# Kernel tuning notes

Hardware: AMD Instinct MI355X
Metric: run time of the kernel (lower is better)

Reference implementation:

```python
import jax, jax.numpy as jnp
import numpy as np

B = 131072  # batch of states
D = 32      # input/hidden width (hardcoded in Policy)
L = 40      # number of hidden layers

def setup_inputs() -> dict:
    key = jax.random.key(0)
    k1, k2, k3, k4, k5 = jax.random.split(key, 5)
    scale = 1.0 / np.sqrt(D)  # ~ torch Linear init scale
    return {
        "state": jax.random.normal(k1, (B, D), dtype=jnp.float32),
        "W_hidden": jax.random.normal(k2, (L, D, D), dtype=jnp.float32) * scale,
        "b_hidden": jax.random.normal(k3, (L, D), dtype=jnp.float32) * scale,
        "W_out": jax.random.normal(k4, (1, D), dtype=jnp.float32) * scale,
        "b_out": jax.random.normal(k5, (1,), dtype=jnp.float32) * scale,
    }

def reference(state, W_hidden, b_hidden, W_out, b_out):
    # torch Linear: y = x @ W.T + b, with W of shape [out, in].
    def layer(x, wb):
        w, b = wb
        return jax.nn.relu(jnp.einsum('bi,oi->bo', x, w) + b), None
    x, _ = jax.lax.scan(layer, state, (W_hidden, b_hidden))
    # final Linear(32, 1), no activation
    return jnp.einsum('bi,oi->bo', x, W_out) + b_out  # [B, 1]
```

## Files before the change

### kernel.cpp

```cpp
#include <hip/hip_runtime.h>


#define NB 131072
#define DD 32
#define NL 40
#define BIAS_BYTES ((NL + 1) * 32 * 4)
#define WTAB_OFF   BIAS_BYTES
#define WTAB_BYTES ((NL + 1) * 4 * 64 * 16)
#define LDS_LAYERS 18
#define LDS_BYTES  (BIAS_BYTES + LDS_LAYERS * 4096)

typedef short bf16x8 __attribute__((ext_vector_type(8)));
typedef float f32x4 __attribute__((ext_vector_type(4)));

union Frag { int4 q; int i[4]; bf16x8 v; };
union BFrag { float4 q; f32x4 v; };

__device__ inline unsigned f2bf(float f) {
  unsigned u = __float_as_uint(f);
  return (u + 0x7fffu + ((u >> 16) & 1u)) >> 16;
}
__device__ inline float bf2f(unsigned s) { return __int_as_float((int)(s << 16)); }

__global__ __launch_bounds__(64) void build_tables(
    const float* __restrict__ Wh, const float* __restrict__ bh,
    const float* __restrict__ Wout, const float* __restrict__ bout,
    char* __restrict__ ws) {
  const int l = blockIdx.x;
  const int lane = threadIdx.x;
  const int m = lane & 15, g = lane >> 4;
  int4* wtab = (int4*)(ws + WTAB_OFF);
  float* bc = (float*)ws;
  for (int p = 0; p < 4; ++p) {
    const int row = (p & 1) ? (16 + m) : m;
    const bool lopart = (p >= 2);
    int wds[4];
    for (int w = 0; w < 4; ++w) {
      unsigned wd = 0;
      for (int e = 0; e < 2; ++e) {
        const int j = 2 * w + e;
        const int k = (j < 4) ? (4 * g + j) : (16 + 4 * g + (j - 4));
        float v;
        if (l < NL) v = Wh[(l * 32 + row) * 32 + k];
        else        v = (row == 0) ? Wout[k] : 0.f;
        unsigned hi = f2bf(v);
        unsigned val = lopart ? f2bf(v - bf2f(hi)) : hi;
        wd |= val << (16 * e);
      }
      wds[w] = (int)wd;
    }
    wtab[(l * 4 + p) * 64 + lane] = make_int4(wds[0], wds[1], wds[2], wds[3]);
  }
  if (lane < 32) {
    float bv = (l < NL) ? bh[l * 32 + lane] : ((lane == 0) ? bout[0] : 0.f);
    bc[l * 32 + lane] = bv;
  }
}

__device__ inline void split2(float a, float b, int& hi, int& lo) {
  const unsigned ia = __float_as_uint(a), ib = __float_as_uint(b);
  hi = (int)__builtin_amdgcn_perm(ia, ib, 0x03020706u);
  const float ha = __int_as_float((int)(ia & 0xffff0000u));
  const float hb = __int_as_float((int)(ib & 0xffff0000u));
  const float la = a - ha, lb = b - hb;
  lo = (int)__builtin_amdgcn_perm(__float_as_uint(la), __float_as_uint(lb),
                                  0x03020706u);
}

#define MFMA16(A, B, C) __builtin_amdgcn_mfma_f32_16x16x32_bf16((A), (B), (C), 0, 0, 0)

__global__ __launch_bounds__(1024, 8) void policy_mfma(
    const float* __restrict__ state, const char* __restrict__ tab,
    float* __restrict__ out) {
  extern __shared__ char smem[];
  const int tid = threadIdx.x;
  const int lane = tid & 63;
  const int n = lane & 15, g = lane >> 4;
  const int wid = blockIdx.x * 16 + (tid >> 6);
  const int bbase = wid * 16;

  {
    const int4* src = (const int4*)tab;
    int4* dst = (int4*)smem;
    for (int i = tid; i < LDS_BYTES / 16; i += 1024) dst[i] = src[i];
  }

  Frag bhi, blo;
  {
    const float* xr = state + (size_t)(bbase + n) * DD;
    float4 xa = *(const float4*)(xr + 4 * g);
    float4 xc = *(const float4*)(xr + 16 + 4 * g);
    split2(xa.x, xa.y, bhi.i[0], blo.i[0]);
    split2(xa.z, xa.w, bhi.i[1], blo.i[1]);
    split2(xc.x, xc.y, bhi.i[2], blo.i[2]);
    split2(xc.z, xc.w, bhi.i[3], blo.i[3]);
  }

  __syncthreads();

  const int4* lw = (const int4*)(smem + WTAB_OFF) + lane;
  const float* bc = (const float*)smem;
  const int4* gw = (const int4*)(tab + WTAB_OFF) + lane;

  auto layer = [&](int l, const int4* __restrict__ WP, int lofs) {
    Frag w0h, w1h, w0l, w1l;
    w0h.q = WP[lofs * 256 + 0];
    w1h.q = WP[lofs * 256 + 64];
    w0l.q = WP[lofs * 256 + 128];
    w1l.q = WP[lofs * 256 + 192];
    BFrag c0, c1;
    c0.q = *(const float4*)(bc + l * 32 + 4 * g);
    c1.q = *(const float4*)(bc + l * 32 + 16 + 4 * g);

    f32x4 a0 = MFMA16(w0h.v, bhi.v, c0.v);
    f32x4 a1 = MFMA16(w1h.v, bhi.v, c1.v);
    a0 = MFMA16(w0l.v, bhi.v, a0);
    a1 = MFMA16(w1l.v, bhi.v, a1);
    a0 = MFMA16(w0h.v, blo.v, a0);
    a1 = MFMA16(w1h.v, blo.v, a1);

    split2(fmaxf(a0[0], 0.f), fmaxf(a0[1], 0.f), bhi.i[0], blo.i[0]);
    split2(fmaxf(a0[2], 0.f), fmaxf(a0[3], 0.f), bhi.i[1], blo.i[1]);
    split2(fmaxf(a1[0], 0.f), fmaxf(a1[1], 0.f), bhi.i[2], blo.i[2]);
    split2(fmaxf(a1[2], 0.f), fmaxf(a1[3], 0.f), bhi.i[3], blo.i[3]);
  };

#pragma unroll
  for (int l = 0; l < LDS_LAYERS; ++l) layer(l, lw, l);
#pragma unroll
  for (int l = LDS_LAYERS; l < NL; ++l) layer(l, gw, l);

  float res;
  {
    Frag w0h, w0l;
    w0h.q = gw[NL * 256 + 0];
    w0l.q = gw[NL * 256 + 128];
    BFrag c0;
    c0.q = *(const float4*)(bc + NL * 32 + 4 * g);
    f32x4 a0 = MFMA16(w0h.v, bhi.v, c0.v);
    a0 = MFMA16(w0l.v, bhi.v, a0);
    a0 = MFMA16(w0h.v, blo.v, a0);
    res = a0[0];
  }

  if (lane < 16) out[bbase + n] = res;
}

extern "C" void kernel_launch(void* const* d_in, const int* in_sizes, int n_in,
                              void* d_out, int out_size, void* d_ws, size_t ws_size,
                              hipStream_t stream) {
  const float* state = (const float*)d_in[0];
  const float* Wh    = (const float*)d_in[1];
  const float* bh    = (const float*)d_in[2];
  const float* Wout  = (const float*)d_in[3];
  const float* bout  = (const float*)d_in[4];
  float* out = (float*)d_out;

  build_tables<<<NL + 1, 64, 0, stream>>>(Wh, bh, Wout, bout, (char*)d_ws);

  policy_mfma<<<512, 1024, LDS_BYTES, stream>>>(state, (const char*)d_ws, out);
}
```

Before: 46.59 us.

## Process four 16-row tiles per wave and stage more layers in LDS

```diff
diff --git a/kernel.cpp b/kernel.cpp
--- a/kernel.cpp
+++ b/kernel.cpp
@@ -7,7 +7,7 @@
 #define BIAS_BYTES ((NL + 1) * 32 * 4)
 #define WTAB_OFF   BIAS_BYTES
 #define WTAB_BYTES ((NL + 1) * 4 * 64 * 16)
-#define LDS_LAYERS 18
+#define LDS_LAYERS 38
 #define LDS_BYTES  (BIAS_BYTES + LDS_LAYERS * 4096)
 
 typedef short bf16x8 __attribute__((ext_vector_type(8)));
@@ -69,31 +69,32 @@
 
 #define MFMA16(A, B, C) __builtin_amdgcn_mfma_f32_16x16x32_bf16((A), (B), (C), 0, 0, 0)
 
-__global__ __launch_bounds__(1024, 8) void policy_mfma(
+__global__ __launch_bounds__(512, 2) void policy_mfma(
     const float* __restrict__ state, const char* __restrict__ tab,
     float* __restrict__ out) {
   extern __shared__ char smem[];
   const int tid = threadIdx.x;
   const int lane = tid & 63;
   const int n = lane & 15, g = lane >> 4;
-  const int wid = blockIdx.x * 16 + (tid >> 6);
-  const int bbase = wid * 16;
+  const int wid = blockIdx.x * 8 + (tid >> 6);
+  const int bbase = wid * 64;
 
   {
     const int4* src = (const int4*)tab;
     int4* dst = (int4*)smem;
-    for (int i = tid; i < LDS_BYTES / 16; i += 1024) dst[i] = src[i];
+    for (int i = tid; i < LDS_BYTES / 16; i += 512) dst[i] = src[i];
   }
 
-  Frag bhi, blo;
-  {
-    const float* xr = state + (size_t)(bbase + n) * DD;
+  Frag bhi[4], blo[4];
+#pragma unroll
+  for (int t = 0; t < 4; ++t) {
+    const float* xr = state + (size_t)(bbase + 16 * t + n) * DD;
     float4 xa = *(const float4*)(xr + 4 * g);
     float4 xc = *(const float4*)(xr + 16 + 4 * g);
-    split2(xa.x, xa.y, bhi.i[0], blo.i[0]);
-    split2(xa.z, xa.w, bhi.i[1], blo.i[1]);
-    split2(xc.x, xc.y, bhi.i[2], blo.i[2]);
-    split2(xc.z, xc.w, bhi.i[3], blo.i[3]);
+    split2(xa.x, xa.y, bhi[t].i[0], blo[t].i[0]);
+    split2(xa.z, xa.w, bhi[t].i[1], blo[t].i[1]);
+    split2(xc.x, xc.y, bhi[t].i[2], blo[t].i[2]);
+    split2(xc.z, xc.w, bhi[t].i[3], blo[t].i[3]);
   }
 
   __syncthreads();
@@ -102,48 +103,63 @@
   const float* bc = (const float*)smem;
   const int4* gw = (const int4*)(tab + WTAB_OFF) + lane;
 
-  auto layer = [&](int l, const int4* __restrict__ WP, int lofs) {
+#pragma unroll
+  for (int l = 0; l < NL; ++l) {
     Frag w0h, w1h, w0l, w1l;
-    w0h.q = WP[lofs * 256 + 0];
-    w1h.q = WP[lofs * 256 + 64];
-    w0l.q = WP[lofs * 256 + 128];
-    w1l.q = WP[lofs * 256 + 192];
+    const int4* WP = (l < LDS_LAYERS) ? lw : gw;
+    w0h.q = WP[l * 256 + 0];
+    w1h.q = WP[l * 256 + 64];
+    w0l.q = WP[l * 256 + 128];
+    w1l.q = WP[l * 256 + 192];
     BFrag c0, c1;
     c0.q = *(const float4*)(bc + l * 32 + 4 * g);
     c1.q = *(const float4*)(bc + l * 32 + 16 + 4 * g);
 
-    f32x4 a0 = MFMA16(w0h.v, bhi.v, c0.v);
-    f32x4 a1 = MFMA16(w1h.v, bhi.v, c1.v);
-    a0 = MFMA16(w0l.v, bhi.v, a0);
-    a1 = MFMA16(w1l.v, bhi.v, a1);
-    a0 = MFMA16(w0h.v, blo.v, a0);
-    a1 = MFMA16(w1h.v, blo.v, a1);
-
-    split2(fmaxf(a0[0], 0.f), fmaxf(a0[1], 0.f), bhi.i[0], blo.i[0]);
-    split2(fmaxf(a0[2], 0.f), fmaxf(a0[3], 0.f), bhi.i[1], blo.i[1]);
-    split2(fmaxf(a1[0], 0.f), fmaxf(a1[1], 0.f), bhi.i[2], blo.i[2]);
-    split2(fmaxf(a1[2], 0.f), fmaxf(a1[3], 0.f), bhi.i[3], blo.i[3]);
-  };
+    f32x4 a0[4], a1[4];
+#pragma unroll
+    for (int t = 0; t < 4; ++t) a0[t] = MFMA16(w0h.v, bhi[t].v, c0.v);
+#pragma unroll
+    for (int t = 0; t < 4; ++t) a1[t] = MFMA16(w1h.v, bhi[t].v, c1.v);
+#pragma unroll
+    for (int t = 0; t < 4; ++t) a0[t] = MFMA16(w0l.v, bhi[t].v, a0[t]);
+#pragma unroll
+    for (int t = 0; t < 4; ++t) a1[t] = MFMA16(w1l.v, bhi[t].v, a1[t]);
+#pragma unroll
+    for (int t = 0; t < 4; ++t) a0[t] = MFMA16(w0h.v, blo[t].v, a0[t]);
+#pragma unroll
+    for (int t = 0; t < 4; ++t) a1[t] = MFMA16(w1h.v, blo[t].v, a1[t]);
 
 #pragma unroll
-  for (int l = 0; l < LDS_LAYERS; ++l) layer(l, lw, l);
-#pragma unroll
-  for (int l = LDS_LAYERS; l < NL; ++l) layer(l, gw, l);
+    for (int t = 0; t < 4; ++t) {
+      split2(fmaxf(a0[t][0], 0.f), fmaxf(a0[t][1], 0.f), bhi[t].i[0], blo[t].i[0]);
+      split2(fmaxf(a0[t][2], 0.f), fmaxf(a0[t][3], 0.f), bhi[t].i[1], blo[t].i[1]);
+      split2(fmaxf(a1[t][0], 0.f), fmaxf(a1[t][1], 0.f), bhi[t].i[2], blo[t].i[2]);
+      split2(fmaxf(a1[t][2], 0.f), fmaxf(a1[t][3], 0.f), bhi[t].i[3], blo[t].i[3]);
+    }
+  }
 
-  float res;
+  float res[4];
   {
     Frag w0h, w0l;
     w0h.q = gw[NL * 256 + 0];
     w0l.q = gw[NL * 256 + 128];
     BFrag c0;
     c0.q = *(const float4*)(bc + NL * 32 + 4 * g);
-    f32x4 a0 = MFMA16(w0h.v, bhi.v, c0.v);
-    a0 = MFMA16(w0l.v, bhi.v, a0);
-    a0 = MFMA16(w0h.v, blo.v, a0);
-    res = a0[0];
+    f32x4 a0[4];
+#pragma unroll
+    for (int t = 0; t < 4; ++t) a0[t] = MFMA16(w0h.v, bhi[t].v, c0.v);
+#pragma unroll
+    for (int t = 0; t < 4; ++t) a0[t] = MFMA16(w0l.v, bhi[t].v, a0[t]);
+#pragma unroll
+    for (int t = 0; t < 4; ++t) a0[t] = MFMA16(w0h.v, blo[t].v, a0[t]);
+#pragma unroll
+    for (int t = 0; t < 4; ++t) res[t] = a0[t][0];
   }
 
-  if (lane < 16) out[bbase + n] = res;
+  if (lane < 16) {
+#pragma unroll
+    for (int t = 0; t < 4; ++t) out[bbase + 16 * t + n] = res[t];
+  }
 }
 
 extern "C" void kernel_launch(void* const* d_in, const int* in_sizes, int n_in,
@@ -158,5 +174,5 @@
 
   build_tables<<<NL + 1, 64, 0, stream>>>(Wh, bh, Wout, bout, (char*)d_ws);
 
-  policy_mfma<<<512, 1024, LDS_BYTES, stream>>>(state, (const char*)d_ws, out);
+  policy_mfma<<<256, 512, LDS_BYTES, stream>>>(state, (const char*)d_ws, out);
 }
```

New measurement: 47.87 us. 1.03x slower.
